# Performance work log

Measured on AMD Instinct MI355X. Metric: run time of the kernel, lower is better.

The kernel has to match this reference:

```python
import jax, jax.numpy as jnp
import numpy as np

B, N, F, E = 2048, 64, 32, 5
U1, U2, UA = 128, 64, 128

def setup_inputs() -> dict:
    key = jax.random.key(0)
    ks = jax.random.split(key, 16)
    inp = {
        'adjacency': jax.random.uniform(ks[0], (B, N, N, E), dtype=jnp.float32),
        'hidden': jnp.zeros((B, 1), dtype=jnp.float32),
        'node': jax.random.normal(ks[1], (B, N, F), dtype=jnp.float32),
        # conv layer 1: per-edge-type dense F->U1 (stacked), plus node dense F->U1
        'W1': jax.random.normal(ks[2], (E - 1, F, U1), dtype=jnp.float32) * 0.05,
        'b1': jnp.zeros((E - 1, U1), dtype=jnp.float32),
        'V1': jax.random.normal(ks[3], (F, U1), dtype=jnp.float32) * 0.05,
        'c1': jnp.zeros((U1,), dtype=jnp.float32),
        # conv layer 2: annotations (U1+F)->U2, node F->U2
        'W2': jax.random.normal(ks[4], (E - 1, U1 + F, U2), dtype=jnp.float32) * 0.05,
        'b2': jnp.zeros((E - 1, U2), dtype=jnp.float32),
        'V2': jax.random.normal(ks[5], (F, U2), dtype=jnp.float32) * 0.05,
        'c2': jnp.zeros((U2,), dtype=jnp.float32),
        # aggregation: (U2+F)->UA gates
        'Wi': jax.random.normal(ks[6], (U2 + F, UA), dtype=jnp.float32) * 0.05,
        'bi': jnp.zeros((UA,), dtype=jnp.float32),
        'Wj': jax.random.normal(ks[7], (U2 + F, UA), dtype=jnp.float32) * 0.05,
        'bj': jnp.zeros((UA,), dtype=jnp.float32),
    }
    return inp


def _gconv(adj_t, annotations, node, W, b, V, c):
    # adj_t: [B,E-1,N,N]; annotations: [B,N,Fa]; node: [B,N,F]
    h = jnp.einsum('bnf,efu->benu', annotations, W) + b[None, :, None, :]
    h = jnp.einsum('bemn,benu->bemu', adj_t, h)          # adjacency-weighted sum
    out = h.sum(axis=1) + node @ V + c                   # [B,N,U]
    return jnp.tanh(out)


def reference(adjacency, hidden, node, W1, b1, V1, c1, W2, b2, V2, c2, Wi, bi, Wj, bj):
    # drop edge type 0, transpose to [B,E-1,N,N]
    adj_t = jnp.transpose(adjacency[:, :, :, 1:], (0, 3, 1, 2))
    # hidden is rank-2 at entry -> first layer uses node only
    h1 = _gconv(adj_t, node, node, W1, b1, V1, c1)                       # [B,N,U1]
    h2 = _gconv(adj_t, jnp.concatenate((h1, node), -1), node, W2, b2, V2, c2)  # [B,N,U2]
    # encoder-level annotations: (output, node) since hidden is rank-2
    ann = jnp.concatenate((h2, node), -1)                                # [B,N,U2+F]
    i = jax.nn.sigmoid(ann @ Wi + bi)
    j = jnp.tanh(ann @ Wj + bj)
    out = jnp.tanh(jnp.sum(i * j, axis=1))                               # [B,UA]
    return out
```

## Files before the change

### kernel.cpp

```cpp
#include <hip/hip_runtime.h>

typedef _Float16 f16;
typedef f16  f16x8 __attribute__((ext_vector_type(8)));
typedef f16  f16x4 __attribute__((ext_vector_type(4)));
typedef float f32x4 __attribute__((ext_vector_type(4)));
typedef unsigned int u32;

#define W1T_HI 0
#define W1T_LO 16384
#define V1T_HI 32768
#define V1T_LO 36864
#define W2T_HI 40960
#define W2T_LO 81920
#define V2T_HI 122880
#define V2T_LO 124928
#define WIT_HI 126976
#define WIT_LO 139264
#define WJT_HI 151552
#define WJT_LO 163840
#define WS_SRC 88064

#define ADJB_HI 0
#define ADJB_LO 32768
#define ANNB_HI 49152
#define ANNB_LO 65536
#define PTB     73728
#define LDS_BYTES 81920

__device__ __forceinline__ f32x4 mfma16(f16x8 a, f16x8 b, f32x4 c){
  return __builtin_amdgcn_mfma_f32_16x16x32_f16(a, b, c, 0, 0, 0);
}
__device__ __forceinline__ float fast_tanh(float x){
  float e = __expf(2.f * x);
  return 1.f - 2.f * __builtin_amdgcn_rcpf(e + 1.f);
}
__device__ __forceinline__ float fast_sigmoid(float x){
  return __builtin_amdgcn_rcpf(1.f + __expf(-x));
}

__device__ __forceinline__ unsigned char enc1(float lo){
  f16 h = (f16)lo;
  unsigned short u = __builtin_bit_cast(unsigned short, h);
  return (unsigned char)(((u32)u + 0x80u) >> 8);
}
__device__ __forceinline__ void enc8(unsigned char* p, const float* lo){
  u32 a = 0, b = 0;
  #pragma unroll
  for (int j = 0; j < 4; ++j) a |= (u32)enc1(lo[j]) << (8*j);
  #pragma unroll
  for (int j = 0; j < 4; ++j) b |= (u32)enc1(lo[4+j]) << (8*j);
  uint2 v = {a, b};
  *(uint2*)p = v;
}
__device__ __forceinline__ u32 enc4(const float* lo){
  return (u32)enc1(lo[0]) | ((u32)enc1(lo[1]) << 8)
       | ((u32)enc1(lo[2]) << 16) | ((u32)enc1(lo[3]) << 24);
}
__device__ __forceinline__ f16x8 dec8(const unsigned char* p){
  uint2 d = *(const uint2*)p;
  u32 w[4];
  w[0] = __builtin_amdgcn_perm(0u, d.x, 0x010c000cu);
  w[1] = __builtin_amdgcn_perm(0u, d.x, 0x030c020cu);
  w[2] = __builtin_amdgcn_perm(0u, d.y, 0x010c000cu);
  w[3] = __builtin_amdgcn_perm(0u, d.y, 0x030c020cu);
  f16x8 r; __builtin_memcpy(&r, w, 16);
  return r;
}

__global__ void prep_weights(const float* __restrict__ W1, const float* __restrict__ V1,
                             const float* __restrict__ W2, const float* __restrict__ V2,
                             const float* __restrict__ Wi, const float* __restrict__ Wj,
                             f16* __restrict__ ws){
  int i = blockIdx.x * 256 + threadIdx.x;
  if (i >= WS_SRC) return;
  float v; int hi_off, lo_off, idx;
  int j = i;
  if (j < 16384){ int e = j >> 12, u = (j >> 5) & 127, f = j & 31;
    v = W1[(e*32 + f)*128 + u]; hi_off = W1T_HI; lo_off = W1T_LO; idx = j; }
  else if ((j -= 16384) < 4096){ int u = j >> 5, f = j & 31;
    v = V1[f*128 + u]; hi_off = V1T_HI; lo_off = V1T_LO; idx = j; }
  else if ((j -= 4096) < 40960){ int e = j / 10240, r = j % 10240, u = r / 160, k = r % 160;
    v = W2[e*10240 + k*64 + u]; hi_off = W2T_HI; lo_off = W2T_LO; idx = j; }
  else if ((j -= 40960) < 2048){ int u = j >> 5, f = j & 31;
    v = V2[f*64 + u]; hi_off = V2T_HI; lo_off = V2T_LO; idx = j; }
  else if ((j -= 2048) < 12288){ int ua = j / 96, k = j % 96;
    v = Wi[k*128 + ua]; hi_off = WIT_HI; lo_off = WIT_LO; idx = j; }
  else { j -= 12288; int ua = j / 96, k = j % 96;
    v = Wj[k*128 + ua]; hi_off = WJT_HI; lo_off = WJT_LO; idx = j; }
  f16 h = (f16)v;
  ws[hi_off + idx] = h;
  ws[lo_off + idx] = (f16)(v - (float)h);
}

__global__ __launch_bounds__(256, 2) void encoder_main(
    const float* __restrict__ adj, const float* __restrict__ node,
    const float* __restrict__ b1, const float* __restrict__ c1,
    const float* __restrict__ b2, const float* __restrict__ c2,
    const float* __restrict__ bi, const float* __restrict__ bj,
    const f16* __restrict__ wb, float* __restrict__ out)
{
  extern __shared__ unsigned char ldsb[];
  f16* adjh            = (f16*)(ldsb + ADJB_HI);
  unsigned char* adjl  = ldsb + ADJB_LO;
  f16* annh            = (f16*)(ldsb + ANNB_HI);
  unsigned char* annl  = ldsb + ANNB_LO;
  unsigned char* ptb   = ldsb + PTB;
  f16* nodeH           = (f16*)(ldsb + PTB);
  f16* nodeLo          = (f16*)(ldsb + PTB + 4096);

  const int tid  = threadIdx.x;
  const int w    = tid >> 6;
  const int lane = tid & 63;
  const int q    = lane >> 4;
  const int l15  = lane & 15;
  const int b    = blockIdx.x;
  const f32x4 z4 = {0.f, 0.f, 0.f, 0.f};

  {
    const float* ap = adj + (size_t)b * 20480;
    #pragma unroll
    for (int i = 0; i < 8; ++i){
      int fu = tid + 256*i;
      int e = fu >> 9, m = (fu >> 3) & 63, uc = fu & 7;
      const float* p = ap + (m*64 + uc*8)*5 + e + 1;
      float v[8], lo[8]; f16x8 hi;
      #pragma unroll
      for (int jj = 0; jj < 8; ++jj) v[jj] = p[jj*5];
      #pragma unroll
      for (int jj = 0; jj < 8; ++jj){
        f16 h = (f16)v[jj]; hi[jj] = h; lo[jj] = v[jj] - (float)h;
      }
      int off = e*4096 + m*64 + ((uc ^ (m & 7)) * 8);
      *(f16x8*)&adjh[off] = hi;
      enc8(&adjl[off], lo);
    }
    const float* np = node + (size_t)b * 2048 + (tid & 63)*32 + (tid >> 6)*8;
    float4 a = *(const float4*)np, c = *(const float4*)(np + 4);
    float v[8] = {a.x, a.y, a.z, a.w, c.x, c.y, c.z, c.w};
    f16x8 hi, lo;
    #pragma unroll
    for (int jj = 0; jj < 8; ++jj){
      f16 h = (f16)v[jj]; hi[jj] = h; lo[jj] = (f16)(v[jj] - (float)h);
    }
    int n = tid & 63, un = tid >> 6;
    *(f16x8*)&nodeH [n*32 + ((un ^ (n & 3)) * 8)] = hi;
    *(f16x8*)&nodeLo[n*32 + ((un ^ (n & 3)) * 8)] = lo;
  }
  __syncthreads();

  f16x8 anh[4], anl[4];
  #pragma unroll
  for (int mt = 0; mt < 4; ++mt){
    anh[mt] = *(const f16x8*)&nodeH [(mt*16 + l15)*32 + ((q ^ (l15 & 3)) * 8)];
    anl[mt] = *(const f16x8*)&nodeLo[(mt*16 + l15)*32 + ((q ^ (l15 & 3)) * 8)];
  }
  __syncthreads();

  const int ptrow  = (w*16 + l15) * 128;
  const int ptlrow = (w*16 + l15) * 128;

  f32x4 acc1[4][2];
  #pragma unroll
  for (int mt = 0; mt < 4; ++mt){ acc1[mt][0] = z4; acc1[mt][1] = z4; }

  #pragma unroll
  for (int e = 0; e < 4; ++e){
    f16x8 ah[2][4], al[2][4];
    #pragma unroll
    for (int ks = 0; ks < 2; ++ks)
      #pragma unroll
      for (int mt = 0; mt < 4; ++mt){
        int off = e*4096 + (mt*16 + l15)*64 + (((ks*4 + q) ^ (l15 & 7)) * 8);
        ah[ks][mt] = *(const f16x8*)&adjh[off];
        al[ks][mt] = dec8(&adjl[off]);
      }
    #pragma unroll
    for (int ut = 0; ut < 2; ++ut){
      const int u = w*32 + ut*16 + l15;
      f16x8 wh = *(const f16x8*)&wb[W1T_HI + (e*128 + u)*32 + q*8];
      f16x8 wl = *(const f16x8*)&wb[W1T_LO + (e*128 + u)*32 + q*8];
      float bias = b1[e*128 + u];
      #pragma unroll
      for (int mt = 0; mt < 4; ++mt){
        f32x4 pf = mfma16(anh[mt], wh, z4);
        pf = mfma16(anl[mt], wh, pf);
        pf = mfma16(anh[mt], wl, pf);
        f16x4 ph; float lo4[4];
        #pragma unroll
        for (int r = 0; r < 4; ++r){
          float v = pf[r] + bias;
          f16 h = (f16)v; ph[r] = h; lo4[r] = v - (float)h;
        }
        int unit = ((mt*2 + (q >> 1)) ^ (l15 & 7));
        *(f16x4*)(ptb + ptrow + unit*16 + (q & 1)*8) = ph;
        *(u32*)(annl + ptlrow + unit*8 + (q & 1)*4) = enc4(lo4);
      }
      #pragma unroll
      for (int ks = 0; ks < 2; ++ks){
        int pu = ((ks*4 + q) ^ (l15 & 7));
        f16x8 bph = *(const f16x8*)(ptb + ptrow + pu*16);
        f16x8 bpl = dec8(annl + ptlrow + pu*8);
        #pragma unroll
        for (int mt = 0; mt < 4; ++mt){
          acc1[mt][ut] = mfma16(ah[ks][mt], bph, acc1[mt][ut]);
          acc1[mt][ut] = mfma16(al[ks][mt], bph, acc1[mt][ut]);
          acc1[mt][ut] = mfma16(ah[ks][mt], bpl, acc1[mt][ut]);
        }
      }
    }
  }
  __syncthreads();

  #pragma unroll
  for (int ut = 0; ut < 2; ++ut){
    const int u = w*32 + ut*16 + l15;
    f16x8 wh = *(const f16x8*)&wb[V1T_HI + u*32 + q*8];
    f16x8 wl = *(const f16x8*)&wb[V1T_LO + u*32 + q*8];
    float cv = c1[u];
    #pragma unroll
    for (int mt = 0; mt < 4; ++mt){
      f32x4 a = acc1[mt][ut];
      a = mfma16(anh[mt], wh, a);
      a = mfma16(anl[mt], wh, a);
      a = mfma16(anh[mt], wl, a);
      #pragma unroll
      for (int r = 0; r < 4; ++r){
        float h = fast_tanh(a[r] + cv);
        f16 hh = (f16)h;
        int row = mt*16 + q*4 + r;
        int unit = ((u >> 3) ^ (row & 7));
        annh[row*128 + unit*8 + (u & 7)] = hh;
        annl[row*128 + unit*8 + (u & 7)] = enc1(h - (float)hh);
      }
    }
  }
  __syncthreads();

  const int u2 = w*16 + l15;
  f32x4 qf[4][4];
  #pragma unroll
  for (int mt = 0; mt < 4; ++mt){
    f16x8 axh[4], axl[4];
    #pragma unroll
    for (int ks = 0; ks < 4; ++ks){
      int off = (mt*16 + l15)*128 + (((ks*4 + q) ^ (l15 & 7)) * 8);
      axh[ks] = *(const f16x8*)&annh[off];
      axl[ks] = dec8(&annl[off]);
    }
    #pragma unroll
    for (int e = 0; e < 4; ++e){
      const f16* w2h = &wb[W2T_HI + (e*64 + u2)*160];
      const f16* w2l = &wb[W2T_LO + (e*64 + u2)*160];
      f16x8 wnh = *(const f16x8*)&w2h[4*32 + q*8];
      f16x8 wnl = *(const f16x8*)&w2l[4*32 + q*8];
      f32x4 t = mfma16(anh[mt], wnh, z4);
      t = mfma16(anl[mt], wnh, t);
      t = mfma16(anh[mt], wnl, t);
      #pragma unroll
      for (int ks = 0; ks < 4; ++ks){
        f16x8 wh = *(const f16x8*)&w2h[ks*32 + q*8];
        f16x8 wl = *(const f16x8*)&w2l[ks*32 + q*8];
        t = mfma16(axh[ks], wh, t);
        t = mfma16(axl[ks], wh, t);
        t = mfma16(axh[ks], wl, t);
      }
      qf[e][mt] = t;
    }
  }
  __syncthreads();

  f32x4 acc2[4];
  #pragma unroll
  for (int mt = 0; mt < 4; ++mt) acc2[mt] = z4;
  #pragma unroll
  for (int e = 0; e < 4; ++e){
    float bias = b2[e*64 + u2];
    #pragma unroll
    for (int mt = 0; mt < 4; ++mt){
      f16x4 ph; float lo4[4];
      #pragma unroll
      for (int r = 0; r < 4; ++r){
        float v = qf[e][mt][r] + bias;
        f16 h = (f16)v; ph[r] = h; lo4[r] = v - (float)h;
      }
      int unit = ((mt*2 + (q >> 1)) ^ (l15 & 7));
      *(f16x4*)(ptb + ptrow + unit*16 + (q & 1)*8) = ph;
      *(u32*)(annl + ptlrow + unit*8 + (q & 1)*4) = enc4(lo4);
    }
    #pragma unroll
    for (int ks = 0; ks < 2; ++ks){
      int pu = ((ks*4 + q) ^ (l15 & 7));
      f16x8 bph = *(const f16x8*)(ptb + ptrow + pu*16);
      f16x8 bpl = dec8(annl + ptlrow + pu*8);
      #pragma unroll
      for (int mt = 0; mt < 4; ++mt){
        int off = e*4096 + (mt*16 + l15)*64 + (((ks*4 + q) ^ (l15 & 7)) * 8);
        f16x8 ah = *(const f16x8*)&adjh[off];
        f16x8 al = dec8(&adjl[off]);
        acc2[mt] = mfma16(ah, bph, acc2[mt]);
        acc2[mt] = mfma16(al, bph, acc2[mt]);
        acc2[mt] = mfma16(ah, bpl, acc2[mt]);
      }
    }
  }
  {
    f16x8 wh = *(const f16x8*)&wb[V2T_HI + u2*32 + q*8];
    f16x8 wl = *(const f16x8*)&wb[V2T_LO + u2*32 + q*8];
    #pragma unroll
    for (int mt = 0; mt < 4; ++mt){
      acc2[mt] = mfma16(anh[mt], wh, acc2[mt]);
      acc2[mt] = mfma16(anl[mt], wh, acc2[mt]);
      acc2[mt] = mfma16(anh[mt], wl, acc2[mt]);
    }
  }
  {
    float cv = c2[u2];
    const int uc = 64 + u2;
    #pragma unroll
    for (int mt = 0; mt < 4; ++mt)
      #pragma unroll
      for (int r = 0; r < 4; ++r){
        float h = fast_tanh(acc2[mt][r] + cv);
        f16 hh = (f16)h;
        int row = mt*16 + q*4 + r;
        int unit = ((uc >> 3) ^ (row & 7));
        annh[row*128 + unit*8 + (uc & 7)] = hh;
        annl[row*128 + unit*8 + (uc & 7)] = enc1(h - (float)hh);
      }
  }
  __syncthreads();

  f16x8 wih[2][3], wil[2][3], wjh[2][3], wjl[2][3];
  float bib[2], bjb[2];
  #pragma unroll
  for (int ut = 0; ut < 2; ++ut){
    const int ua = w*32 + ut*16 + l15;
    #pragma unroll
    for (int ks = 0; ks < 3; ++ks){
      wih[ut][ks] = *(const f16x8*)&wb[WIT_HI + ua*96 + ks*32 + q*8];
      wil[ut][ks] = *(const f16x8*)&wb[WIT_LO + ua*96 + ks*32 + q*8];
      wjh[ut][ks] = *(const f16x8*)&wb[WJT_HI + ua*96 + ks*32 + q*8];
      wjl[ut][ks] = *(const f16x8*)&wb[WJT_LO + ua*96 + ks*32 + q*8];
    }
    bib[ut] = bi[ua]; bjb[ut] = bj[ua];
  }
  float s[2] = {0.f, 0.f};
  #pragma unroll
  for (int mt = 0; mt < 4; ++mt){
    f16x8 gh[2], gl[2];
    #pragma unroll
    for (int ks = 0; ks < 2; ++ks){
      int off = (mt*16 + l15)*128 + (((8 + ks*4 + q) ^ (l15 & 7)) * 8);
      gh[ks] = *(const f16x8*)&annh[off];
      gl[ks] = dec8(&annl[off]);
    }
    #pragma unroll
    for (int ut = 0; ut < 2; ++ut){
      f32x4 ia = mfma16(anh[mt], wih[ut][2], z4);
      ia = mfma16(anl[mt], wih[ut][2], ia);
      ia = mfma16(anh[mt], wil[ut][2], ia);
      f32x4 ja = mfma16(anh[mt], wjh[ut][2], z4);
      ja = mfma16(anl[mt], wjh[ut][2], ja);
      ja = mfma16(anh[mt], wjl[ut][2], ja);
      #pragma unroll
      for (int ks = 0; ks < 2; ++ks){
        ia = mfma16(gh[ks], wih[ut][ks], ia);
        ia = mfma16(gl[ks], wih[ut][ks], ia);
        ia = mfma16(gh[ks], wil[ut][ks], ia);
        ja = mfma16(gh[ks], wjh[ut][ks], ja);
        ja = mfma16(gl[ks], wjh[ut][ks], ja);
        ja = mfma16(gh[ks], wjl[ut][ks], ja);
      }
      #pragma unroll
      for (int r = 0; r < 4; ++r)
        s[ut] += fast_sigmoid(ia[r] + bib[ut]) * fast_tanh(ja[r] + bjb[ut]);
    }
  }
  #pragma unroll
  for (int ut = 0; ut < 2; ++ut){
    float t = s[ut];
    t += __shfl_xor(t, 16);
    t += __shfl_xor(t, 32);
    if (q == 0) out[(size_t)b*128 + (w*32 + ut*16 + l15)] = fast_tanh(t);
  }
}

extern "C" void kernel_launch(void* const* d_in, const int* in_sizes, int n_in,
                              void* d_out, int out_size, void* d_ws, size_t ws_size,
                              hipStream_t stream) {
  (void)in_sizes; (void)n_in; (void)out_size; (void)ws_size;
  const float* adj  = (const float*)d_in[0];
  const float* node = (const float*)d_in[2];
  const float* W1   = (const float*)d_in[3];
  const float* b1   = (const float*)d_in[4];
  const float* V1   = (const float*)d_in[5];
  const float* c1   = (const float*)d_in[6];
  const float* W2   = (const float*)d_in[7];
  const float* b2   = (const float*)d_in[8];
  const float* V2   = (const float*)d_in[9];
  const float* c2   = (const float*)d_in[10];
  const float* Wi   = (const float*)d_in[11];
  const float* bi   = (const float*)d_in[12];
  const float* Wj   = (const float*)d_in[13];
  const float* bj   = (const float*)d_in[14];
  f16* wb    = (f16*)d_ws;
  float* out = (float*)d_out;

  hipFuncSetAttribute((const void*)encoder_main,
                      hipFuncAttributeMaxDynamicSharedMemorySize, LDS_BYTES);

  prep_weights<<<(WS_SRC + 255) / 256, 256, 0, stream>>>(W1, V1, W2, V2, Wi, Wj, wb);
  encoder_main<<<2048, 256, LDS_BYTES, stream>>>(adj, node, b1, c1, b2, c2, bi, bj, wb, out);
}
```

Before: 367.4 us.

## Store adjacency and annotations as 16-bit fixed point in LDS

Adjacency values and tanh annotations are stored in LDS as 16-bit unsigned fixed-point codes. They are decoded into hi/lo f16 pairs with bit tricks, replacing the separate f16-hi plus 8-bit-lo buffers. This shrinks the LDS footprint from 80KB to 48KB so launch bounds can go to 3 blocks per CU. The adjacency global load is rewritten as contiguous float4 reads, and an extra barrier is added because the buffers now alias. This trades some precision (16-bit fixed point rather than roughly 19 bits) and decode ALU work for higher occupancy and coalesced loads.

```diff
diff --git a/kernel.cpp b/kernel.cpp
--- a/kernel.cpp
+++ b/kernel.cpp
@@ -3,8 +3,11 @@
 typedef _Float16 f16;
 typedef f16  f16x8 __attribute__((ext_vector_type(8)));
 typedef f16  f16x4 __attribute__((ext_vector_type(4)));
+typedef f16  f16x2v __attribute__((ext_vector_type(2)));
 typedef float f32x4 __attribute__((ext_vector_type(4)));
 typedef unsigned int u32;
+typedef unsigned short u16;
+typedef unsigned char u8;
 
 #define W1T_HI 0
 #define W1T_LO 16384
@@ -20,12 +23,7 @@
 #define WJT_LO 163840
 #define WS_SRC 88064
 
-#define ADJB_HI 0
-#define ADJB_LO 32768
-#define ANNB_HI 49152
-#define ANNB_LO 65536
-#define PTB     73728
-#define LDS_BYTES 81920
+#define LDS_BYTES 49152
 
 __device__ __forceinline__ f32x4 mfma16(f16x8 a, f16x8 b, f32x4 c){
   return __builtin_amdgcn_mfma_f32_16x16x32_f16(a, b, c, 0, 0, 0);
@@ -38,25 +36,39 @@
   return __builtin_amdgcn_rcpf(1.f + __expf(-x));
 }
 
-__device__ __forceinline__ unsigned char enc1(float lo){
+__device__ __forceinline__ void dec_q16(uint4 d, u32 orh, f16 ch, u32 orl, f16 cl,
+                                        f16x8& hi, f16x8& lo){
+  u32 dd[4] = {d.x, d.y, d.z, d.w};
+  f16x2v hv[4], lv[4];
+  #pragma unroll
+  for (int i = 0; i < 4; ++i){
+    u32 hb = ((dd[i] >> 6) & 0x03FF03FFu) | orh;
+    u32 lb = ((dd[i] << 4) & 0x03F003F0u) | orl;
+    hv[i] = __builtin_bit_cast(f16x2v, hb) + (f16x2v){ch, ch};
+    lv[i] = __builtin_bit_cast(f16x2v, lb) + (f16x2v){cl, cl};
+  }
+  __builtin_memcpy(&hi, hv, 16);
+  __builtin_memcpy(&lo, lv, 16);
+}
+#define AORH 0x3C003C00u
+#define AORL 0x14001400u
+#define NORH 0x40004000u
+#define NORL 0x18001800u
+#define ACH ((f16)(-1.0f))
+#define ACL ((f16)(-0.0009765625f))
+#define NCH ((f16)(-3.0f))
+#define NCL ((f16)(-0.001953125f))
+
+__device__ __forceinline__ u8 enc1(float lo){
   f16 h = (f16)lo;
   unsigned short u = __builtin_bit_cast(unsigned short, h);
-  return (unsigned char)(((u32)u + 0x80u) >> 8);
-}
-__device__ __forceinline__ void enc8(unsigned char* p, const float* lo){
-  u32 a = 0, b = 0;
-  #pragma unroll
-  for (int j = 0; j < 4; ++j) a |= (u32)enc1(lo[j]) << (8*j);
-  #pragma unroll
-  for (int j = 0; j < 4; ++j) b |= (u32)enc1(lo[4+j]) << (8*j);
-  uint2 v = {a, b};
-  *(uint2*)p = v;
+  return (u8)(((u32)u + 0x80u) >> 8);
 }
 __device__ __forceinline__ u32 enc4(const float* lo){
   return (u32)enc1(lo[0]) | ((u32)enc1(lo[1]) << 8)
        | ((u32)enc1(lo[2]) << 16) | ((u32)enc1(lo[3]) << 24);
 }
-__device__ __forceinline__ f16x8 dec8(const unsigned char* p){
+__device__ __forceinline__ f16x8 dec8(const u8* p){
   uint2 d = *(const uint2*)p;
   u32 w[4];
   w[0] = __builtin_amdgcn_perm(0u, d.x, 0x010c000cu);
@@ -92,21 +104,19 @@
   ws[lo_off + idx] = (f16)(v - (float)h);
 }
 
-__global__ __launch_bounds__(256, 2) void encoder_main(
+__global__ __launch_bounds__(256, 3) void encoder_main(
     const float* __restrict__ adj, const float* __restrict__ node,
     const float* __restrict__ b1, const float* __restrict__ c1,
     const float* __restrict__ b2, const float* __restrict__ c2,
     const float* __restrict__ bi, const float* __restrict__ bj,
     const f16* __restrict__ wb, float* __restrict__ out)
 {
-  extern __shared__ unsigned char ldsb[];
-  f16* adjh            = (f16*)(ldsb + ADJB_HI);
-  unsigned char* adjl  = ldsb + ADJB_LO;
-  f16* annh            = (f16*)(ldsb + ANNB_HI);
-  unsigned char* annl  = ldsb + ANNB_LO;
-  unsigned char* ptb   = ldsb + PTB;
-  f16* nodeH           = (f16*)(ldsb + PTB);
-  f16* nodeLo          = (f16*)(ldsb + PTB + 4096);
+  extern __shared__ u8 ldsb[];
+  u16* adjq   = (u16*)ldsb;
+  u16* annq   = (u16*)(ldsb + 32768);
+  u8*  ptb    = ldsb + 32768;
+  f16* nodeH  = (f16*)(ldsb + 32768);
+  f16* nodeLo = (f16*)(ldsb + 32768 + 4096);
 
   const int tid  = threadIdx.x;
   const int w    = tid >> 6;
@@ -117,22 +127,26 @@
   const f32x4 z4 = {0.f, 0.f, 0.f, 0.f};
 
   {
-    const float* ap = adj + (size_t)b * 20480;
-    #pragma unroll
-    for (int i = 0; i < 8; ++i){
-      int fu = tid + 256*i;
-      int e = fu >> 9, m = (fu >> 3) & 63, uc = fu & 7;
-      const float* p = ap + (m*64 + uc*8)*5 + e + 1;
-      float v[8], lo[8]; f16x8 hi;
-      #pragma unroll
-      for (int jj = 0; jj < 8; ++jj) v[jj] = p[jj*5];
-      #pragma unroll
-      for (int jj = 0; jj < 8; ++jj){
-        f16 h = (f16)v[jj]; hi[jj] = h; lo[jj] = v[jj] - (float)h;
-      }
-      int off = e*4096 + m*64 + ((uc ^ (m & 7)) * 8);
-      *(f16x8*)&adjh[off] = hi;
-      enc8(&adjl[off], lo);
+    const float4* ap = (const float4*)(adj + (size_t)b * 20480) + tid*20;
+    const int m  = tid >> 2, q2 = tid & 3;
+    const int mo = m * 64;
+    #pragma unroll
+    for (int half = 0; half < 2; ++half){
+      float4 fl[10];
+      #pragma unroll
+      for (int i = 0; i < 10; ++i) fl[i] = ap[half*10 + i];
+      #pragma unroll
+      for (int c8 = 0; c8 < 8; ++c8){
+        int c = half*8 + c8;
+        int unit = ((q2*2 + (c >> 3)) ^ (m & 7));
+        int base = mo + unit*8 + (c & 7);
+        #pragma unroll
+        for (int ef = 1; ef <= 4; ++ef){
+          float v = ((const float*)fl)[c8*5 + ef];
+          u32 k = (u32)(v * 65536.f);
+          adjq[(ef-1)*4096 + base] = (u16)k;
+        }
+      }
     }
     const float* np = node + (size_t)b * 2048 + (tid & 63)*32 + (tid >> 6)*8;
     float4 a = *(const float4*)np, c = *(const float4*)(np + 4);
@@ -156,8 +170,7 @@
   }
   __syncthreads();
 
-  const int ptrow  = (w*16 + l15) * 128;
-  const int ptlrow = (w*16 + l15) * 128;
+  const int ptrow = (w*16 + l15) * 256;
 
   f32x4 acc1[4][2];
   #pragma unroll
@@ -170,9 +183,9 @@
     for (int ks = 0; ks < 2; ++ks)
       #pragma unroll
       for (int mt = 0; mt < 4; ++mt){
-        int off = e*4096 + (mt*16 + l15)*64 + (((ks*4 + q) ^ (l15 & 7)) * 8);
-        ah[ks][mt] = *(const f16x8*)&adjh[off];
-        al[ks][mt] = dec8(&adjl[off]);
+        uint4 d = *(const uint4*)&adjq[e*4096 + (mt*16 + l15)*64
+                                       + (((ks*4 + q) ^ (l15 & 7)) * 8)];
+        dec_q16(d, AORH, ACH, AORL, ACL, ah[ks][mt], al[ks][mt]);
       }
     #pragma unroll
     for (int ut = 0; ut < 2; ++ut){
@@ -193,13 +206,13 @@
         }
         int unit = ((mt*2 + (q >> 1)) ^ (l15 & 7));
         *(f16x4*)(ptb + ptrow + unit*16 + (q & 1)*8) = ph;
-        *(u32*)(annl + ptlrow + unit*8 + (q & 1)*4) = enc4(lo4);
+        *(u32*)(ptb + ptrow + 128 + unit*8 + (q & 1)*4) = enc4(lo4);
       }
       #pragma unroll
       for (int ks = 0; ks < 2; ++ks){
         int pu = ((ks*4 + q) ^ (l15 & 7));
         f16x8 bph = *(const f16x8*)(ptb + ptrow + pu*16);
-        f16x8 bpl = dec8(annl + ptlrow + pu*8);
+        f16x8 bpl = dec8(ptb + ptrow + 128 + pu*8);
         #pragma unroll
         for (int mt = 0; mt < 4; ++mt){
           acc1[mt][ut] = mfma16(ah[ks][mt], bph, acc1[mt][ut]);
@@ -226,11 +239,10 @@
       #pragma unroll
       for (int r = 0; r < 4; ++r){
         float h = fast_tanh(a[r] + cv);
-        f16 hh = (f16)h;
+        u32 k = (u32)((h + 1.f) * 32768.f);
+        k = k > 65535u ? 65535u : k;
         int row = mt*16 + q*4 + r;
-        int unit = ((u >> 3) ^ (row & 7));
-        annh[row*128 + unit*8 + (u & 7)] = hh;
-        annl[row*128 + unit*8 + (u & 7)] = enc1(h - (float)hh);
+        annq[row*128 + (((u >> 3) ^ (row & 7)) * 8) + (u & 7)] = (u16)k;
       }
     }
   }
@@ -243,9 +255,9 @@
     f16x8 axh[4], axl[4];
     #pragma unroll
     for (int ks = 0; ks < 4; ++ks){
-      int off = (mt*16 + l15)*128 + (((ks*4 + q) ^ (l15 & 7)) * 8);
-      axh[ks] = *(const f16x8*)&annh[off];
-      axl[ks] = dec8(&annl[off]);
+      uint4 d = *(const uint4*)&annq[(mt*16 + l15)*128
+                                     + (((ks*4 + q) ^ (l15 & 7)) * 8)];
+      dec_q16(d, NORH, NCH, NORL, NCL, axh[ks], axl[ks]);
     }
     #pragma unroll
     for (int e = 0; e < 4; ++e){
@@ -285,18 +297,18 @@
       }
       int unit = ((mt*2 + (q >> 1)) ^ (l15 & 7));
       *(f16x4*)(ptb + ptrow + unit*16 + (q & 1)*8) = ph;
-      *(u32*)(annl + ptlrow + unit*8 + (q & 1)*4) = enc4(lo4);
+      *(u32*)(ptb + ptrow + 128 + unit*8 + (q & 1)*4) = enc4(lo4);
     }
     #pragma unroll
     for (int ks = 0; ks < 2; ++ks){
       int pu = ((ks*4 + q) ^ (l15 & 7));
       f16x8 bph = *(const f16x8*)(ptb + ptrow + pu*16);
-      f16x8 bpl = dec8(annl + ptlrow + pu*8);
+      f16x8 bpl = dec8(ptb + ptrow + 128 + pu*8);
       #pragma unroll
       for (int mt = 0; mt < 4; ++mt){
-        int off = e*4096 + (mt*16 + l15)*64 + (((ks*4 + q) ^ (l15 & 7)) * 8);
-        f16x8 ah = *(const f16x8*)&adjh[off];
-        f16x8 al = dec8(&adjl[off]);
+        uint4 d = *(const uint4*)&adjq[e*4096 + (mt*16 + l15)*64 + pu*8];
+        f16x8 ah, al;
+        dec_q16(d, AORH, ACH, AORL, ACL, ah, al);
         acc2[mt] = mfma16(ah, bph, acc2[mt]);
         acc2[mt] = mfma16(al, bph, acc2[mt]);
         acc2[mt] = mfma16(ah, bpl, acc2[mt]);
@@ -313,6 +325,7 @@
       acc2[mt] = mfma16(anh[mt], wl, acc2[mt]);
     }
   }
+  __syncthreads();
   {
     float cv = c2[u2];
     const int uc = 64 + u2;
@@ -321,11 +334,10 @@
       #pragma unroll
       for (int r = 0; r < 4; ++r){
         float h = fast_tanh(acc2[mt][r] + cv);
-        f16 hh = (f16)h;
+        u32 k = (u32)((h + 1.f) * 32768.f);
+        k = k > 65535u ? 65535u : k;
         int row = mt*16 + q*4 + r;
-        int unit = ((uc >> 3) ^ (row & 7));
-        annh[row*128 + unit*8 + (uc & 7)] = hh;
-        annl[row*128 + unit*8 + (uc & 7)] = enc1(h - (float)hh);
+        annq[row*128 + (((uc >> 3) ^ (row & 7)) * 8) + (uc & 7)] = (u16)k;
       }
   }
   __syncthreads();
@@ -350,9 +362,9 @@
     f16x8 gh[2], gl[2];
     #pragma unroll
     for (int ks = 0; ks < 2; ++ks){
-      int off = (mt*16 + l15)*128 + (((8 + ks*4 + q) ^ (l15 & 7)) * 8);
-      gh[ks] = *(const f16x8*)&annh[off];
-      gl[ks] = dec8(&annl[off]);
+      uint4 d = *(const uint4*)&annq[(mt*16 + l15)*128
+                                     + (((8 + ks*4 + q) ^ (l15 & 7)) * 8)];
+      dec_q16(d, NORH, NCH, NORL, NCL, gh[ks], gl[ks]);
     }
     #pragma unroll
     for (int ut = 0; ut < 2; ++ut){
```

Result: slower. 410.1 us (+11.6%).
